# Optimization experiments

Measured on AMD Instinct MI355X. Metric: run time of the kernel, lower is better.

The kernel has to match this reference:

```python
import jax, jax.numpy as jnp
import numpy as np

N_NODES = 100000
N_EDGES = 1600000
D_IN = 64
D_OUT = 64


def setup_inputs() -> dict:
    key = jax.random.key(0)
    ks = jax.random.split(key, 8)
    x = jax.random.normal(ks[0], (N_NODES, D_IN), dtype=jnp.float32)
    edge_rows = jax.random.randint(ks[1], (N_EDGES,), 0, N_NODES, dtype=jnp.int32)
    edge_cols = jax.random.randint(ks[2], (N_EDGES,), 0, N_NODES, dtype=jnp.int32)
    edge_vals = jax.random.uniform(ks[3], (N_EDGES,), dtype=jnp.float32)
    # xavier_uniform with gain=2.0: limit = gain * sqrt(6 / (fan_in + fan_out))
    lim = 2.0 * float(np.sqrt(6.0 / (D_IN + D_OUT)))
    weight_own = jax.random.uniform(ks[4], (D_IN, D_OUT), jnp.float32, -lim, lim)
    weight_nbr = jax.random.uniform(ks[5], (D_IN, D_OUT), jnp.float32, -lim, lim)
    weight_temp = jax.random.uniform(ks[6], (D_IN, D_OUT), jnp.float32, -lim, lim)
    bias = jnp.zeros((D_OUT,), jnp.float32)
    return {
        "x": x,
        "edge_rows": edge_rows,
        "edge_cols": edge_cols,
        "edge_vals": edge_vals,
        "weight_own": weight_own,
        "weight_nbr": weight_nbr,
        "weight_temp": weight_temp,
        "bias": bias,
    }


def _spmm(edge_rows, edge_cols, edge_vals, dense):
    # COO sparse [N,N] @ dense [N,D]: gather source rows, scale by edge value,
    # scatter-add into destination rows.
    msgs = edge_vals[:, None] * dense[edge_cols]  # [E, D]
    return jax.ops.segment_sum(msgs, edge_rows, num_segments=N_NODES)


def reference(x, edge_rows, edge_cols, edge_vals, weight_own, weight_nbr, weight_temp, bias):
    support = x @ weight_own    # [N, D_OUT]
    support1 = x @ weight_nbr
    support2 = x @ weight_temp
    output = _spmm(edge_rows, edge_cols, edge_vals, support)
    output1 = _spmm(edge_rows, edge_cols, edge_vals, support1)
    output2 = _spmm(edge_rows, edge_cols, edge_vals, support2)
    return output + output1 + output2 + bias
```

## Files before the change

### kernel.cpp

```cpp
#include <hip/hip_runtime.h>
#include <hip/hip_bf16.h>

#define D 64
#define RPB 1024
#define RSH 10
#define NBB 128
#define CPAD 16

__global__ __launch_bounds__(256) void gemm_kernel(const float* __restrict__ x,
                                                   const float* __restrict__ w0,
                                                   const float* __restrict__ w1,
                                                   const float* __restrict__ w2,
                                                   __hip_bfloat16* __restrict__ support,
                                                   int n) {
    __shared__ float Ws[D * D];
    __shared__ float xs[4][D];

    for (int i = threadIdx.x; i < D * D; i += 256)
        Ws[i] = w0[i] + w1[i] + w2[i];
    __syncthreads();

    const int wid  = threadIdx.x >> 6;
    const int lane = threadIdx.x & 63;
    int row = blockIdx.x * 4 + wid;
    const int nw = gridDim.x * 4;

    for (; row < n; row += nw) {
        xs[wid][lane] = x[(size_t)row * D + lane];
        float acc = 0.0f;
#pragma unroll
        for (int k = 0; k < D; ++k) {
            acc += xs[wid][k] * Ws[k * D + lane];
        }
        support[(size_t)row * D + lane] = __float2bfloat16(acc);
    }
}

__global__ __launch_bounds__(256) void gemm_f32_kernel(const float* __restrict__ x,
                                                       const float* __restrict__ w0,
                                                       const float* __restrict__ w1,
                                                       const float* __restrict__ w2,
                                                       float* __restrict__ support,
                                                       int n) {
    __shared__ float Ws[D * D];
    __shared__ float xs[4][D];
    for (int i = threadIdx.x; i < D * D; i += 256)
        Ws[i] = w0[i] + w1[i] + w2[i];
    __syncthreads();
    const int wid  = threadIdx.x >> 6;
    const int lane = threadIdx.x & 63;
    int row = blockIdx.x * 4 + wid;
    const int nw = gridDim.x * 4;
    for (; row < n; row += nw) {
        xs[wid][lane] = x[(size_t)row * D + lane];
        float acc = 0.0f;
#pragma unroll
        for (int k = 0; k < D; ++k) acc += xs[wid][k] * Ws[k * D + lane];
        support[(size_t)row * D + lane] = acc;
    }
}

__global__ __launch_bounds__(256) void zero_kernel(int* __restrict__ p, int n) {
    int i = blockIdx.x * 256 + threadIdx.x;
    int stride = gridDim.x * 256;
    for (; i < n; i += stride) p[i] = 0;
}

__global__ __launch_bounds__(256) void bucket_hist_kernel(const int* __restrict__ rows,
                                                          int ne, int* __restrict__ gcnt,
                                                          int nb) {
    __shared__ int lcnt[NBB];
    for (int i = threadIdx.x; i < nb; i += 256) lcnt[i] = 0;
    __syncthreads();
    int i = blockIdx.x * 256 + threadIdx.x;
    int stride = gridDim.x * 256;
    for (; i < ne; i += stride) atomicAdd(&lcnt[rows[i] >> RSH], 1);
    __syncthreads();
    for (int b = threadIdx.x; b < nb; b += 256) {
        int c = lcnt[b];
        if (c) atomicAdd(&gcnt[b * CPAD], c);
    }
}

__global__ __launch_bounds__(256) void bucket_scan_kernel(const int* __restrict__ gcnt,
                                                          int nb,
                                                          int* __restrict__ base,
                                                          int* __restrict__ cursor,
                                                          int* __restrict__ rowptr,
                                                          int n) {
    __shared__ int ts[256];
    const int tid = threadIdx.x;
    int v = (tid < nb) ? gcnt[tid * CPAD] : 0;
    ts[tid] = v;
    __syncthreads();
    for (int off = 1; off < 256; off <<= 1) {
        int t = (tid >= off) ? ts[tid - off] : 0;
        __syncthreads();
        ts[tid] += t;
        __syncthreads();
    }
    int excl = ts[tid] - v;
    if (tid < nb) { base[tid] = excl; cursor[tid * CPAD] = excl; }
    if (tid == 255) { base[nb] = ts[255]; rowptr[n] = ts[255]; }
}

__global__ __launch_bounds__(256) void bin_scatter_kernel(const int* __restrict__ rows,
                                                          const int* __restrict__ cols,
                                                          const float* __restrict__ vals,
                                                          int ne,
                                                          int* __restrict__ cursor,
                                                          int nb,
                                                          int2* __restrict__ binned) {
    __shared__ int lcnt[NBB];
    __shared__ int lbase[NBB];
    const int tid = threadIdx.x;
    const int ce = (ne + gridDim.x - 1) / gridDim.x;
    const int e0 = blockIdx.x * ce;
    const int e1 = min(ne, e0 + ce);

    for (int i = tid; i < nb; i += 256) lcnt[i] = 0;
    __syncthreads();
    for (int e = e0 + tid; e < e1; e += 256) atomicAdd(&lcnt[rows[e] >> RSH], 1);
    __syncthreads();
    for (int b = tid; b < nb; b += 256) {
        int c = lcnt[b];
        lbase[b] = c ? atomicAdd(&cursor[b * CPAD], c) : 0;
    }
    __syncthreads();
    for (int i = tid; i < nb; i += 256) lcnt[i] = 0;
    __syncthreads();
    for (int e = e0 + tid; e < e1; e += 256) {
        int r = rows[e];
        int b = r >> RSH;
        int loc = atomicAdd(&lcnt[b], 1);
        int2 cv;
        cv.x = ((r & (RPB - 1)) << 17) | cols[e];
        cv.y = __float_as_int(vals[e]);
        binned[lbase[b] + loc] = cv;
    }
}

__global__ __launch_bounds__(512) void local_csr_kernel(const int* __restrict__ base,
                                                        const int2* __restrict__ binned,
                                                        int* __restrict__ rowptr,
                                                        int2* __restrict__ csr,
                                                        int n) {
    __shared__ int lh[RPB];
    __shared__ int ts[512];
    const int tid = threadIdx.x;
    const int b = blockIdx.x >> 2;
    const int q = blockIdx.x & 3;
    const int jb = base[b], je = base[b + 1];

    lh[2 * tid] = 0; lh[2 * tid + 1] = 0;
    __syncthreads();
    for (int j = jb + tid; j < je; j += 512)
        atomicAdd(&lh[binned[j].x >> 17], 1);
    __syncthreads();

    const int v0 = lh[2 * tid], v1 = lh[2 * tid + 1];
    const int tsum = v0 + v1;
    ts[tid] = tsum;
    __syncthreads();
    for (int off = 1; off < 512; off <<= 1) {
        int t = (tid >= off) ? ts[tid - off] : 0;
        __syncthreads();
        ts[tid] += t;
        __syncthreads();
    }
    int excl = ts[tid] - tsum + jb;
    __syncthreads();

    const int r0 = b * RPB + 2 * tid;
    lh[2 * tid] = excl;
    if (r0 < n) rowptr[r0] = excl;
    lh[2 * tid + 1] = excl + v0;
    if (r0 + 1 < n) rowptr[r0 + 1] = excl + v0;
    __syncthreads();

    for (int j = jb + tid; j < je; j += 512) {
        int2 e = binned[j];
        int rl = e.x >> 17;
        if ((rl >> 8) == q) {
            int pos = atomicAdd(&lh[rl], 1);
            int2 o; o.x = e.x & 0x1FFFF; o.y = e.y;
            csr[pos] = o;
        }
    }
}

__global__ __launch_bounds__(256) void pull2_kernel(const int* __restrict__ rowptr,
                                                    const int2* __restrict__ csr,
                                                    const unsigned int* __restrict__ sup32,
                                                    const float* __restrict__ bias,
                                                    float* __restrict__ out, int n) {
    const int tid  = threadIdx.x;
    const int lane = tid & 63;
    const int half = lane >> 5;
    const int sub  = lane & 31;
    const int wave = blockIdx.x * 4 + (tid >> 6);
    const int nwave = gridDim.x * 4;
    const float2 b2 = reinterpret_cast<const float2*>(bias)[sub];

    for (int w = wave; 2 * w < n; w += nwave) {
        const int r = 2 * w + half;
        float ax = 0.0f, ay = 0.0f;
        if (r < n) {
            const int jb = rowptr[r], je = rowptr[r + 1];
            int j = jb;
            for (; j + 7 < je; j += 8) {
                int2 e[8];
#pragma unroll
                for (int u = 0; u < 8; ++u) e[u] = csr[j + u];
                unsigned int g[8];
#pragma unroll
                for (int u = 0; u < 8; ++u)
                    g[u] = sup32[(size_t)e[u].x * 32 + sub];
#pragma unroll
                for (int u = 0; u < 8; ++u) {
                    float v = __int_as_float(e[u].y);
                    ax += v * __uint_as_float(g[u] << 16);
                    ay += v * __uint_as_float(g[u] & 0xffff0000u);
                }
            }
            for (; j + 1 < je; j += 2) {
                int2 e0 = csr[j], e1 = csr[j + 1];
                unsigned int u0 = sup32[(size_t)e0.x * 32 + sub];
                unsigned int u1 = sup32[(size_t)e1.x * 32 + sub];
                float v0 = __int_as_float(e0.y), v1 = __int_as_float(e1.y);
                ax += v0 * __uint_as_float(u0 << 16);
                ay += v0 * __uint_as_float(u0 & 0xffff0000u);
                ax += v1 * __uint_as_float(u1 << 16);
                ay += v1 * __uint_as_float(u1 & 0xffff0000u);
            }
            if (j < je) {
                int2 e = csr[j];
                unsigned int u = sup32[(size_t)e.x * 32 + sub];
                float v = __int_as_float(e.y);
                ax += v * __uint_as_float(u << 16);
                ay += v * __uint_as_float(u & 0xffff0000u);
            }
            float2 o; o.x = ax + b2.x; o.y = ay + b2.y;
            reinterpret_cast<float2*>(out)[(size_t)r * 32 + sub] = o;
        }
    }
}

__global__ __launch_bounds__(256) void init_kernel(const float* __restrict__ bias,
                                                   float* __restrict__ out, int total4) {
    int i = blockIdx.x * 256 + threadIdx.x;
    int stride = gridDim.x * 256;
    for (; i < total4; i += stride) {
        int base4 = (i * 4) & (D - 1);
        float4 bv;
        bv.x = bias[base4 + 0]; bv.y = bias[base4 + 1];
        bv.z = bias[base4 + 2]; bv.w = bias[base4 + 3];
        reinterpret_cast<float4*>(out)[i] = bv;
    }
}

__global__ __launch_bounds__(256) void scatter_kernel(const int* __restrict__ rows,
                                                      const int* __restrict__ cols,
                                                      const float* __restrict__ vals,
                                                      const float* __restrict__ support,
                                                      float* __restrict__ out, int ne) {
    const int wid  = blockIdx.x * 4 + (threadIdx.x >> 6);
    const int lane = threadIdx.x & 63;
    const int nw = gridDim.x * 4;
    for (int e = wid; e < ne; e += nw) {
        const int r = rows[e];
        const int c = cols[e];
        const float v = vals[e];
        unsafeAtomicAdd(&out[(size_t)r * D + lane], v * support[(size_t)c * D + lane]);
    }
}

extern "C" void kernel_launch(void* const* d_in, const int* in_sizes, int n_in,
                              void* d_out, int out_size, void* d_ws, size_t ws_size,
                              hipStream_t stream) {
    const float* x         = (const float*)d_in[0];
    const int*   edge_rows = (const int*)d_in[1];
    const int*   edge_cols = (const int*)d_in[2];
    const float* edge_vals = (const float*)d_in[3];
    const float* w_own     = (const float*)d_in[4];
    const float* w_nbr     = (const float*)d_in[5];
    const float* w_temp    = (const float*)d_in[6];
    const float* bias      = (const float*)d_in[7];

    float* out = (float*)d_out;
    const int n_nodes = in_sizes[0] / D;
    const int n_edges = in_sizes[1];
    const int nb = (n_nodes + RPB - 1) / RPB;

    char* ws = (char*)d_ws;
    size_t off = 0;
    auto take = [&](size_t bytes) -> char* {
        char* p = ws + off;
        off = (off + bytes + 15) & ~(size_t)15;
        return p;
    };
    __hip_bfloat16* support = (__hip_bfloat16*)take((size_t)n_nodes * D * sizeof(__hip_bfloat16));
    int2* binned = (int2*)take((size_t)n_edges * sizeof(int2));
    int2* csr    = (int2*)take((size_t)n_edges * sizeof(int2));
    int*  rowptr = (int*) take((size_t)(n_nodes + 1) * sizeof(int));
    int*  gcnt   = (int*) take((size_t)nb * CPAD * sizeof(int));
    int*  base   = (int*) take((size_t)(nb + 1) * sizeof(int));
    int*  cursor = (int*) take((size_t)nb * CPAD * sizeof(int));
    const bool full_fits = (off <= ws_size) && (nb <= NBB) && (n_nodes <= (1 << 17));

    if (full_fits) {
        gemm_kernel<<<1024, 256, 0, stream>>>(x, w_own, w_nbr, w_temp, support, n_nodes);
        zero_kernel<<<8, 256, 0, stream>>>(gcnt, nb * CPAD);
        bucket_hist_kernel<<<512, 256, 0, stream>>>(edge_rows, n_edges, gcnt, nb);
        bucket_scan_kernel<<<1, 256, 0, stream>>>(gcnt, nb, base, cursor, rowptr, n_nodes);
        bin_scatter_kernel<<<512, 256, 0, stream>>>(edge_rows, edge_cols, edge_vals,
                                                    n_edges, cursor, nb, binned);
        local_csr_kernel<<<nb * 4, 512, 0, stream>>>(base, binned, rowptr, csr, n_nodes);
        pull2_kernel<<<2048, 256, 0, stream>>>(rowptr, csr, (const unsigned int*)support,
                                               bias, out, n_nodes);
    } else {
        float* support_f = (float*)d_ws;
        gemm_f32_kernel<<<1024, 256, 0, stream>>>(x, w_own, w_nbr, w_temp, support_f, n_nodes);
        int total4 = (n_nodes * D) / 4;
        int blocks = (total4 + 255) / 256; if (blocks > 2048) blocks = 2048;
        init_kernel<<<blocks, 256, 0, stream>>>(bias, out, total4);
        scatter_kernel<<<2048, 256, 0, stream>>>(edge_rows, edge_cols, edge_vals,
                                                 support_f, out, n_edges);
    }
}
```

Before: 138.7 us.

## Fuse GEMM into bin-scatter kernel via block specialization to overlap stages

Merges the dense x·(W_own+W_nbr+W_temp) GEMM and the edge bin-scatter pass into one launch, with the first 512 blocks doing the scatter and the remaining 2048 blocks doing the GEMM. This removes a separate kernel launch and lets the compute-bound GEMM overlap with the memory/atomic-bound scatter. The GEMM grid also grows from 1024 to 2048 blocks. Each block now reserves shared memory for both roles, which may reduce occupancy for the scatter blocks.

Result: faster. 132.8 us (median of 2 runs) (-4.2%).

```diff
diff --git a/kernel.cpp b/kernel.cpp
--- a/kernel.cpp
+++ b/kernel.cpp
@@ -6,33 +6,62 @@
 #define RSH 10
 #define NBB 128
 #define CPAD 16
-
-__global__ __launch_bounds__(256) void gemm_kernel(const float* __restrict__ x,
-                                                   const float* __restrict__ w0,
-                                                   const float* __restrict__ w1,
-                                                   const float* __restrict__ w2,
-                                                   __hip_bfloat16* __restrict__ support,
-                                                   int n) {
+#define NSB 512
+
+__global__ __launch_bounds__(256) void fused_scatter_gemm_kernel(
+        const int* __restrict__ rows, const int* __restrict__ cols,
+        const float* __restrict__ vals, int ne,
+        int* __restrict__ cursor, int nb, int2* __restrict__ binned,
+        const float* __restrict__ x, const float* __restrict__ w0,
+        const float* __restrict__ w1, const float* __restrict__ w2,
+        __hip_bfloat16* __restrict__ support, int n) {
     __shared__ float Ws[D * D];
     __shared__ float xs[4][D];
-
-    for (int i = threadIdx.x; i < D * D; i += 256)
-        Ws[i] = w0[i] + w1[i] + w2[i];
-    __syncthreads();
-
-    const int wid  = threadIdx.x >> 6;
-    const int lane = threadIdx.x & 63;
-    int row = blockIdx.x * 4 + wid;
-    const int nw = gridDim.x * 4;
-
-    for (; row < n; row += nw) {
-        xs[wid][lane] = x[(size_t)row * D + lane];
-        float acc = 0.0f;
-#pragma unroll
-        for (int k = 0; k < D; ++k) {
-            acc += xs[wid][k] * Ws[k * D + lane];
-        }
-        support[(size_t)row * D + lane] = __float2bfloat16(acc);
+    __shared__ int lcnt[NBB];
+    __shared__ int lbase[NBB];
+    const int tid = threadIdx.x;
+
+    if (blockIdx.x < NSB) {
+        const int ce = (ne + NSB - 1) / NSB;
+        const int e0 = blockIdx.x * ce;
+        const int e1 = min(ne, e0 + ce);
+
+        for (int i = tid; i < nb; i += 256) lcnt[i] = 0;
+        __syncthreads();
+        for (int e = e0 + tid; e < e1; e += 256) atomicAdd(&lcnt[rows[e] >> RSH], 1);
+        __syncthreads();
+        for (int b = tid; b < nb; b += 256) {
+            int c = lcnt[b];
+            lbase[b] = c ? atomicAdd(&cursor[b * CPAD], c) : 0;
+        }
+        __syncthreads();
+        for (int i = tid; i < nb; i += 256) lcnt[i] = 0;
+        __syncthreads();
+        for (int e = e0 + tid; e < e1; e += 256) {
+            int r = rows[e];
+            int b = r >> RSH;
+            int loc = atomicAdd(&lcnt[b], 1);
+            int2 cv;
+            cv.x = ((r & (RPB - 1)) << 17) | cols[e];
+            cv.y = __float_as_int(vals[e]);
+            binned[lbase[b] + loc] = cv;
+        }
+    } else {
+        for (int i = tid; i < D * D; i += 256)
+            Ws[i] = w0[i] + w1[i] + w2[i];
+        __syncthreads();
+        const int wid  = tid >> 6;
+        const int lane = tid & 63;
+        const int gb = blockIdx.x - NSB;
+        int row = gb * 4 + wid;
+        const int nw = (gridDim.x - NSB) * 4;
+        for (; row < n; row += nw) {
+            xs[wid][lane] = x[(size_t)row * D + lane];
+            float acc = 0.0f;
+#pragma unroll
+            for (int k = 0; k < D; ++k) acc += xs[wid][k] * Ws[k * D + lane];
+            support[(size_t)row * D + lane] = __float2bfloat16(acc);
+        }
     }
 }
 
@@ -102,42 +131,6 @@
     int excl = ts[tid] - v;
     if (tid < nb) { base[tid] = excl; cursor[tid * CPAD] = excl; }
     if (tid == 255) { base[nb] = ts[255]; rowptr[n] = ts[255]; }
-}
-
-__global__ __launch_bounds__(256) void bin_scatter_kernel(const int* __restrict__ rows,
-                                                          const int* __restrict__ cols,
-                                                          const float* __restrict__ vals,
-                                                          int ne,
-                                                          int* __restrict__ cursor,
-                                                          int nb,
-                                                          int2* __restrict__ binned) {
-    __shared__ int lcnt[NBB];
-    __shared__ int lbase[NBB];
-    const int tid = threadIdx.x;
-    const int ce = (ne + gridDim.x - 1) / gridDim.x;
-    const int e0 = blockIdx.x * ce;
-    const int e1 = min(ne, e0 + ce);
-
-    for (int i = tid; i < nb; i += 256) lcnt[i] = 0;
-    __syncthreads();
-    for (int e = e0 + tid; e < e1; e += 256) atomicAdd(&lcnt[rows[e] >> RSH], 1);
-    __syncthreads();
-    for (int b = tid; b < nb; b += 256) {
-        int c = lcnt[b];
-        lbase[b] = c ? atomicAdd(&cursor[b * CPAD], c) : 0;
-    }
-    __syncthreads();
-    for (int i = tid; i < nb; i += 256) lcnt[i] = 0;
-    __syncthreads();
-    for (int e = e0 + tid; e < e1; e += 256) {
-        int r = rows[e];
-        int b = r >> RSH;
-        int loc = atomicAdd(&lcnt[b], 1);
-        int2 cv;
-        cv.x = ((r & (RPB - 1)) << 17) | cols[e];
-        cv.y = __float_as_int(vals[e]);
-        binned[lbase[b] + loc] = cv;
-    }
 }
 
 __global__ __launch_bounds__(512) void local_csr_kernel(const int* __restrict__ base,
@@ -309,12 +302,12 @@
     const bool full_fits = (off <= ws_size) && (nb <= NBB) && (n_nodes <= (1 << 17));
 
     if (full_fits) {
-        gemm_kernel<<<1024, 256, 0, stream>>>(x, w_own, w_nbr, w_temp, support, n_nodes);
         zero_kernel<<<8, 256, 0, stream>>>(gcnt, nb * CPAD);
         bucket_hist_kernel<<<512, 256, 0, stream>>>(edge_rows, n_edges, gcnt, nb);
         bucket_scan_kernel<<<1, 256, 0, stream>>>(gcnt, nb, base, cursor, rowptr, n_nodes);
-        bin_scatter_kernel<<<512, 256, 0, stream>>>(edge_rows, edge_cols, edge_vals,
-                                                    n_edges, cursor, nb, binned);
+        fused_scatter_gemm_kernel<<<NSB + 2048, 256, 0, stream>>>(
+            edge_rows, edge_cols, edge_vals, n_edges, cursor, nb, binned,
+            x, w_own, w_nbr, w_temp, support, n_nodes);
         local_csr_kernel<<<nb * 4, 512, 0, stream>>>(base, binned, rowptr, csr, n_nodes);
         pull2_kernel<<<2048, 256, 0, stream>>>(rowptr, csr, (const unsigned int*)support,
                                                bias, out, n_nodes);
```
